# Optimization experiments

Measured on AMD Instinct MI355X. Metric: run time of the kernel, lower is better.

Reference implementation:

```python
import jax, jax.numpy as jnp
import numpy as np

MAX_SEQ_LEN = 4096

def bigbird_block_rand_mask(from_seq_length, to_seq_length, from_block_size, to_block_size, num_rand_blocks, last_idx=-1):
    rand_attn = np.zeros((from_seq_length // from_block_size - 2, num_rand_blocks), dtype=np.int32)
    middle_seq = np.arange(1, to_seq_length // to_block_size - 1, dtype=np.int32)
    last = to_seq_length // to_block_size - 1
    if last_idx > 2 * to_block_size:
        last = last_idx // to_block_size - 1
    r = num_rand_blocks
    nfb = from_seq_length // from_block_size
    for i in range(1, nfb - 1):
        start = i - 2
        end = i
        if i == 1:
            rand_attn[i - 1, :] = np.random.permutation(middle_seq[2:last])[:r]
        elif i == 2:
            rand_attn[i - 1, :] = np.random.permutation(middle_seq[3:last])[:r]
        elif i == nfb - 3:
            rand_attn[i - 1, :] = np.random.permutation(middle_seq[:last])[:r]
        elif i == nfb - 2:
            rand_attn[i - 1, :] = np.random.permutation(middle_seq[:last])[:r]
        elif start > last:
            start = last
            rand_attn[i - 1, :] = np.random.permutation(middle_seq[:start])[:r]
        elif end + 1 == last:
            rand_attn[i - 1, :] = np.random.permutation(middle_seq[:start])[:r]
        else:
            rand_attn[i - 1, :] = np.random.permutation(np.concatenate((middle_seq[:start], middle_seq[end + 1:last])))[:r]
    return rand_attn

def full_bigbird_mask(from_seq_length, to_seq_length, from_block_size, to_block_size, rand_attn):
    attn_mask = np.zeros((MAX_SEQ_LEN, MAX_SEQ_LEN), dtype=np.int32)
    for i in range(1, from_seq_length // from_block_size - 1):
        attn_mask[i * from_block_size:(i + 1) * from_block_size, (i - 1) * to_block_size:(i + 2) * to_block_size] = 1
        for j in rand_attn[i - 1, :]:
            attn_mask[i * from_block_size:(i + 1) * from_block_size, j * to_block_size:(j + 1) * to_block_size] = 1
    attn_mask[:from_block_size, :] = 1
    attn_mask[:, :to_block_size] = 1
    attn_mask[:, -to_block_size:] = 1
    attn_mask[-from_block_size:, :] = 1
    return attn_mask[:from_seq_length, :to_seq_length].astype(bool)

def setup_inputs() -> dict:
    B, H, F, T, D = 2, 16, 1024, 1024, 64
    BS, R, SEED = 64, 3, 0
    np.random.seed(SEED)
    rand_attn = np.stack([
        bigbird_block_rand_mask(MAX_SEQ_LEN, MAX_SEQ_LEN, BS, BS, R, last_idx=1024)[:F // BS - 2]
        for _ in range(H)
    ], axis=0)
    mask = np.stack([full_bigbird_mask(F, T, BS, BS, rand_attn[h]) for h in range(H)], axis=0)
    attention_mask = jnp.asarray(mask[None].astype(np.float32))  # [1, H, F, T]
    key = jax.random.key(0)
    kq, kk, kv = jax.random.split(key, 3)
    return {
        'query_layer': jax.random.normal(kq, (B, H, F, D), dtype=jnp.float32),
        'key_layer': jax.random.normal(kk, (B, H, T, D), dtype=jnp.float32),
        'value_layer': jax.random.normal(kv, (B, H, T, D), dtype=jnp.float32),
        'attention_mask': attention_mask,
    }

def reference(query_layer, key_layer, value_layer, attention_mask):
    d = query_layer.shape[-1]
    scores = jnp.einsum('bnfh,bnth->bnft', query_layer, key_layer) * (1.0 / np.sqrt(float(d)))
    scores = scores + (1.0 - attention_mask) * -10000.0
    probs = jax.nn.softmax(scores, axis=-1)
    # [batch, from_seq, heads, size_per_head]
    return jnp.einsum('bnft,bnth->bfnh', probs, value_layer)
```

## Files before the change

kernel.cpp:

```cpp
#include <hip/hip_runtime.h>

typedef __attribute__((ext_vector_type(4))) float f32x4;
typedef __attribute__((ext_vector_type(8))) short bf16x8;
typedef _Float16 f16x8 __attribute__((ext_vector_type(8)));

#define MFMA16(a, b, c) __builtin_amdgcn_mfma_f32_16x16x32_f16((a), (b), (c), 0, 0, 0)
#define MFMABF(a, b, c) __builtin_amdgcn_mfma_f32_16x16x32_bf16((a), (b), (c), 0, 0, 0)

constexpr size_t TILE_FRAG_BYTES = 8192;
constexpr size_t NTILES = 512;
constexpr size_t ARR_S  = NTILES * TILE_FRAG_BYTES;
constexpr size_t WS_NEED = 2 * ARR_S;

__device__ __forceinline__ int swz_off(int row, int col) {
    return (row * 128 + col * 2) ^ ((row & 7) << 4);
}
__device__ __forceinline__ f16x8 ld_frag16(const char* tile, int row, int col) {
    return *(const f16x8*)(tile + swz_off(row, col));
}

__global__ __launch_bounds__(256) void bigbird_prepass(
    const float* __restrict__ K, const float* __restrict__ V,
    char* __restrict__ ws) {
    __shared__ float vf[64][66];
    const int tile = blockIdx.x;
    const int tid  = threadIdx.x;
    const float* Kt = K + (size_t)tile * 4096;
    const float* Vt = V + (size_t)tile * 4096;
    f16x8* Ko = (f16x8*)(ws + (size_t)tile * TILE_FRAG_BYTES);
    f16x8* Vo = (f16x8*)(ws + ARR_S + (size_t)tile * TILE_FRAG_BYTES);

    {
        const int row = tid >> 2;
        const int c0  = (tid & 3) << 4;
        const float* p = Vt + row * 64 + c0;
        f32x4 e0 = *(const f32x4*)p,       e1 = *(const f32x4*)(p + 4),
              e2 = *(const f32x4*)(p + 8), e3 = *(const f32x4*)(p + 12);
#pragma unroll
        for (int e = 0; e < 4; ++e) {
            vf[row][c0 + e] = e0[e];     vf[row][c0 + 4 + e] = e1[e];
            vf[row][c0 + 8 + e] = e2[e]; vf[row][c0 + 12 + e] = e3[e];
        }
    }
#pragma unroll
    for (int t = 0; t < 2; ++t) {
        int s = tid + t * 256;
        int f = s >> 6, lane = s & 63;
        int j = f >> 1, kk = f & 1;
        int l16 = lane & 15, g = lane >> 4;
        const float* p = Kt + (j * 16 + l16) * 64 + kk * 32 + g * 8;
        f32x4 a = *(const f32x4*)p;
        f32x4 c = *(const f32x4*)(p + 4);
        f16x8 kv;
#pragma unroll
        for (int e = 0; e < 4; ++e) {
            kv[e]     = (_Float16)a[e];
            kv[4 + e] = (_Float16)c[e];
        }
        Ko[s] = kv;
    }
    __syncthreads();
#pragma unroll
    for (int t = 0; t < 2; ++t) {
        int s = tid + t * 256;
        int f = s >> 6, lane = s & 63;
        int j = f >> 1, kk = f & 1;
        int l16 = lane & 15, g = lane >> 4;
        f16x8 vv;
#pragma unroll
        for (int e = 0; e < 8; ++e)
            vv[e] = (_Float16)vf[kk * 32 + g * 8 + e][j * 16 + l16];
        Vo[s] = vv;
    }
}

__global__ __launch_bounds__(256, 2) void bigbird_main(
    const float* __restrict__ Q, const float* __restrict__ M,
    const char* __restrict__ ws, float* __restrict__ Out) {
    constexpr int H = 16, F = 1024, D = 64;

    __shared__ char fbuf[2][16384];
    __shared__ char p_sm[4][2048];
    __shared__ int flags[16];
    __shared__ int list[16];
    __shared__ int ncnt;

    const int i0  = blockIdx.x;
    const int xcd = i0 & 7;
    const int q0  = i0 >> 3;
    const int grp = xcd * 4 + (q0 >> 4);
    const int fb  = q0 & 15;
    const int b   = grp >> 4;
    const int h   = grp & 15;
    const int bh  = grp;

    const int tid  = threadIdx.x;
    const int lane = tid & 63;
    const int w    = tid >> 6;
    const int g    = lane >> 4;
    const int l16  = lane & 15;

    if (tid < 16)
        flags[tid] = (M[((size_t)(h * 1024 + fb * 64)) * 1024 + tid * 64] > 0.5f) ? 1 : 0;

    f16x8 qf[2];
    {
        const float* qr = Q + ((size_t)bh * F + fb * 64 + w * 16 + l16) * D;
#pragma unroll
        for (int kk = 0; kk < 2; ++kk) {
            const float* p = qr + kk * 32 + g * 8;
            f32x4 a = *(const f32x4*)p;
            f32x4 c = *(const f32x4*)(p + 4);
#pragma unroll
            for (int e = 0; e < 8; ++e)
                qf[kk][e] = (_Float16)((e < 4 ? a[e] : c[e - 4]) * 0.125f);
        }
    }
    __syncthreads();
    if (tid == 0) {
        int nn = 0;
        for (int t = 0; t < 16; ++t)
            if (flags[t]) list[nn++] = t;
        ncnt = nn;
    }
    __syncthreads();
    const int n = ncnt;

    f32x4 acc[4];
    float m_r[4], l_r[4];
#pragma unroll
    for (int j = 0; j < 4; ++j) acc[j] = f32x4{0.f, 0.f, 0.f, 0.f};
#pragma unroll
    for (int r = 0; r < 4; ++r) { m_r[r] = -1e30f; l_r[r] = 0.f; }

    const char* wsK = ws + (size_t)bh * 16 * TILE_FRAG_BYTES;
    const char* wsV = wsK + ARR_S;
    char* pw = p_sm[w];

    auto stage = [&](int bufi, int tb) {
        const char* Kt = wsK + (size_t)tb * TILE_FRAG_BYTES;
        const char* Vt = wsV + (size_t)tb * TILE_FRAG_BYTES;
        char* dst = fbuf[bufi] + w * 1024;
#pragma unroll
        for (int c = 0; c < 4; ++c) {
            const char* src = (c < 2 ? Kt + c * 4096 : Vt + (c - 2) * 4096) + tid * 16;
            __builtin_amdgcn_global_load_lds(
                (const __attribute__((address_space(1))) void*)src,
                (__attribute__((address_space(3))) void*)(dst + c * 4096), 16, 0, 0);
        }
    };

    if (n > 0) stage(0, list[0]);

    for (int i = 0; i < n; ++i) {
        __syncthreads();
        if (i + 1 < n) stage((i + 1) & 1, list[i + 1]);
        const char* Kb = fbuf[i & 1];
        const char* Vb = fbuf[i & 1] + 8192;

        f32x4 s[4];
#pragma unroll
        for (int j = 0; j < 4; ++j) {
            s[j] = f32x4{0.f, 0.f, 0.f, 0.f};
#pragma unroll
            for (int kk = 0; kk < 2; ++kk) {
                f16x8 kf = *(const f16x8*)(Kb + (j * 2 + kk) * 1024 + lane * 16);
                s[j] = MFMA16(qf[kk], kf, s[j]);
            }
        }

        float rmax[4];
#pragma unroll
        for (int r = 0; r < 4; ++r)
            rmax[r] = fmaxf(fmaxf(s[0][r], s[1][r]), fmaxf(s[2][r], s[3][r]));
#pragma unroll
        for (int off = 1; off < 16; off <<= 1)
#pragma unroll
            for (int r = 0; r < 4; ++r)
                rmax[r] = fmaxf(rmax[r], __shfl_xor(rmax[r], off, 64));
        float alpha[4], psum[4];
#pragma unroll
        for (int r = 0; r < 4; ++r) {
            float mn = fmaxf(m_r[r], rmax[r]);
            alpha[r] = __expf(m_r[r] - mn);
            m_r[r]   = mn;
            psum[r]  = 0.f;
        }
#pragma unroll
        for (int j = 0; j < 4; ++j)
#pragma unroll
            for (int r = 0; r < 4; ++r) {
                float pe = __expf(s[j][r] - m_r[r]);
                s[j][r] = pe;
                psum[r] += pe;
            }
#pragma unroll
        for (int off = 1; off < 16; off <<= 1)
#pragma unroll
            for (int r = 0; r < 4; ++r)
                psum[r] += __shfl_xor(psum[r], off, 64);
#pragma unroll
        for (int r = 0; r < 4; ++r)
            l_r[r] = l_r[r] * alpha[r] + psum[r];
#pragma unroll
        for (int j = 0; j < 4; ++j)
#pragma unroll
            for (int r = 0; r < 4; ++r)
                acc[j][r] *= alpha[r];

#pragma unroll
        for (int j = 0; j < 4; ++j)
#pragma unroll
            for (int r = 0; r < 4; ++r)
                *(_Float16*)(pw + swz_off(g * 4 + r, j * 16 + l16)) = (_Float16)s[j][r];
        asm volatile("s_waitcnt lgkmcnt(0)" ::: "memory");
        __builtin_amdgcn_sched_barrier(0);

#pragma unroll
        for (int kk = 0; kk < 2; ++kk) {
            f16x8 pa = ld_frag16(pw, l16, kk * 32 + g * 8);
#pragma unroll
            for (int jd = 0; jd < 4; ++jd) {
                f16x8 vfr = *(const f16x8*)(Vb + (jd * 2 + kk) * 1024 + lane * 16);
                acc[jd] = MFMA16(pa, vfr, acc[jd]);
            }
        }
    }

#pragma unroll
    for (int r = 0; r < 4; ++r) {
        float inv = 1.0f / l_r[r];
        int f = fb * 64 + w * 16 + g * 4 + r;
        float* ob = Out + ((size_t)(b * F + f) * H + h) * D;
#pragma unroll
        for (int jd = 0; jd < 4; ++jd)
            ob[jd * 16 + l16] = acc[jd][r] * inv;
    }
}

__device__ __forceinline__ unsigned short f2bf(float x) {
    unsigned u = __builtin_bit_cast(unsigned, x);
    unsigned r = u + 0x7fffu + ((u >> 16) & 1u);
    return (unsigned short)(r >> 16);
}
__device__ __forceinline__ float bf2f(unsigned short h) {
    return __builtin_bit_cast(float, (unsigned)h << 16);
}
__device__ __forceinline__ bf16x8 ld_fragb(const char* tile, int row, int col) {
    return *(const bf16x8*)(tile + swz_off(row, col));
}
__device__ __forceinline__ void stage_rm_fb(const float* __restrict__ src,
                                            char* hi_t, char* lo_t, float scale) {
    const int tid = threadIdx.x;
    const int row = tid >> 2;
    const int c0  = (tid & 3) << 4;
    const float* p = src + row * 64 + c0;
    f32x4 vv[4] = { *(const f32x4*)(p), *(const f32x4*)(p + 4),
                    *(const f32x4*)(p + 8), *(const f32x4*)(p + 12) };
    bf16x8 h2[2], l2[2];
#pragma unroll
    for (int e = 0; e < 16; ++e) {
        float x = vv[e >> 2][e & 3] * scale;
        unsigned short hb = f2bf(x);
        unsigned short lb = f2bf(x - bf2f(hb));
        h2[e >> 3][e & 7] = (short)hb;
        l2[e >> 3][e & 7] = (short)lb;
    }
#pragma unroll
    for (int gi = 0; gi < 2; ++gi) {
        int off = swz_off(row, c0 + gi * 8);
        *(bf16x8*)(hi_t + off) = h2[gi];
        *(bf16x8*)(lo_t + off) = l2[gi];
    }
}
__device__ __forceinline__ void stage_tr_fb(const float* __restrict__ src,
                                            char* hi_t, char* lo_t) {
    const int tid = threadIdx.x;
    const int t  = tid >> 2;
    const int c0 = (tid & 3) << 4;
    const float* p = src + t * 64 + c0;
    f32x4 vv[4] = { *(const f32x4*)(p), *(const f32x4*)(p + 4),
                    *(const f32x4*)(p + 8), *(const f32x4*)(p + 12) };
#pragma unroll
    for (int e = 0; e < 16; ++e) {
        float x = vv[e >> 2][e & 3];
        unsigned short hb = f2bf(x);
        unsigned short lb = f2bf(x - bf2f(hb));
        int d = c0 + e;
        int off = (d * 128 + t * 2) ^ ((d & 7) << 4);
        *(unsigned short*)(hi_t + off) = hb;
        *(unsigned short*)(lo_t + off) = lb;
    }
}
__global__ __launch_bounds__(256) void bigbird_kernel_fb(
    const float* __restrict__ Q, const float* __restrict__ K,
    const float* __restrict__ V, const float* __restrict__ M,
    float* __restrict__ Out) {
    constexpr int H = 16, F = 1024, D = 64;
    __shared__ char kq_hi[8192];
    __shared__ char kq_lo[8192];
    __shared__ char vt_hi[8192];
    __shared__ char vt_lo[8192];
    __shared__ char p_smf[8192];
    __shared__ int flags[16];
    const int bid = blockIdx.x;
    const int fb  = bid & 15;
    const int h   = (bid >> 4) & 15;
    const int b   = bid >> 8;
    const int tid  = threadIdx.x;
    const int lane = tid & 63;
    const int w    = tid >> 6;
    const int g    = lane >> 4;
    const int l16  = lane & 15;
    if (tid < 16)
        flags[tid] = (M[(h * 1024 + fb * 64) * 1024 + tid * 64] > 0.5f) ? 1 : 0;
    const float* qb = Q + ((size_t)(b * H + h) * F + fb * 64) * D;
    stage_rm_fb(qb, kq_hi, kq_lo, 0.125f);
    __syncthreads();
    bf16x8 qh[2], ql[2];
#pragma unroll
    for (int kk = 0; kk < 2; ++kk) {
        qh[kk] = ld_fragb(kq_hi, w * 16 + l16, kk * 32 + g * 8);
        ql[kk] = ld_fragb(kq_lo, w * 16 + l16, kk * 32 + g * 8);
    }
    f32x4 acc[4];
    float m_r[4], l_r[4];
#pragma unroll
    for (int j = 0; j < 4; ++j) acc[j] = f32x4{0.f, 0.f, 0.f, 0.f};
#pragma unroll
    for (int r = 0; r < 4; ++r) { m_r[r] = -1e30f; l_r[r] = 0.f; }
    const float* kb = K + (size_t)(b * H + h) * 1024 * D;
    const float* vb = V + (size_t)(b * H + h) * 1024 * D;
    for (int tb = 0; tb < 16; ++tb) {
        if (!flags[tb]) continue;
        __syncthreads();
        stage_rm_fb(kb + tb * 64 * D, kq_hi, kq_lo, 1.0f);
        stage_tr_fb(vb + tb * 64 * D, vt_hi, vt_lo);
        __syncthreads();
        f32x4 s[4];
#pragma unroll
        for (int j = 0; j < 4; ++j) {
            s[j] = f32x4{0.f, 0.f, 0.f, 0.f};
#pragma unroll
            for (int kk = 0; kk < 2; ++kk) {
                bf16x8 bhf = ld_fragb(kq_hi, j * 16 + l16, kk * 32 + g * 8);
                bf16x8 blf = ld_fragb(kq_lo, j * 16 + l16, kk * 32 + g * 8);
                s[j] = MFMABF(qh[kk], bhf, s[j]);
                s[j] = MFMABF(qh[kk], blf, s[j]);
                s[j] = MFMABF(ql[kk], bhf, s[j]);
            }
        }
        float rmax[4];
#pragma unroll
        for (int r = 0; r < 4; ++r)
            rmax[r] = fmaxf(fmaxf(s[0][r], s[1][r]), fmaxf(s[2][r], s[3][r]));
#pragma unroll
        for (int off = 1; off < 16; off <<= 1)
#pragma unroll
            for (int r = 0; r < 4; ++r)
                rmax[r] = fmaxf(rmax[r], __shfl_xor(rmax[r], off, 64));
        float alpha[4], psum[4];
#pragma unroll
        for (int r = 0; r < 4; ++r) {
            float mn = fmaxf(m_r[r], rmax[r]);
            alpha[r] = __expf(m_r[r] - mn);
            m_r[r]   = mn;
            psum[r]  = 0.f;
        }
#pragma unroll
        for (int j = 0; j < 4; ++j)
#pragma unroll
            for (int r = 0; r < 4; ++r) {
                float pe = __expf(s[j][r] - m_r[r]);
                s[j][r] = pe;
                psum[r] += pe;
            }
#pragma unroll
        for (int off = 1; off < 16; off <<= 1)
#pragma unroll
            for (int r = 0; r < 4; ++r)
                psum[r] += __shfl_xor(psum[r], off, 64);
#pragma unroll
        for (int r = 0; r < 4; ++r)
            l_r[r] = l_r[r] * alpha[r] + psum[r];
#pragma unroll
        for (int j = 0; j < 4; ++j)
#pragma unroll
            for (int r = 0; r < 4; ++r)
                acc[j][r] *= alpha[r];
#pragma unroll
        for (int j = 0; j < 4; ++j)
#pragma unroll
            for (int r = 0; r < 4; ++r) {
                int row = w * 16 + g * 4 + r;
                *(unsigned short*)(p_smf + swz_off(row, j * 16 + l16)) = f2bf(s[j][r]);
            }
        __syncthreads();
#pragma unroll
        for (int kk = 0; kk < 2; ++kk) {
            bf16x8 pa = ld_fragb(p_smf, w * 16 + l16, kk * 32 + g * 8);
#pragma unroll
            for (int jd = 0; jd < 4; ++jd) {
                bf16x8 vh = ld_fragb(vt_hi, jd * 16 + l16, kk * 32 + g * 8);
                bf16x8 vl = ld_fragb(vt_lo, jd * 16 + l16, kk * 32 + g * 8);
                acc[jd] = MFMABF(pa, vh, acc[jd]);
                acc[jd] = MFMABF(pa, vl, acc[jd]);
            }
        }
    }
#pragma unroll
    for (int r = 0; r < 4; ++r) {
        float inv = 1.0f / l_r[r];
        int f = fb * 64 + w * 16 + g * 4 + r;
        float* ob = Out + ((size_t)(b * F + f) * H + h) * D;
#pragma unroll
        for (int jd = 0; jd < 4; ++jd)
            ob[jd * 16 + l16] = acc[jd][r] * inv;
    }
}

extern "C" void kernel_launch(void* const* d_in, const int* in_sizes, int n_in,
                              void* d_out, int out_size, void* d_ws, size_t ws_size,
                              hipStream_t stream) {
    const float* q = (const float*)d_in[0];
    const float* k = (const float*)d_in[1];
    const float* v = (const float*)d_in[2];
    const float* m = (const float*)d_in[3];
    float* out = (float*)d_out;
    if (ws_size >= WS_NEED) {
        bigbird_prepass<<<dim3(512), dim3(256), 0, stream>>>(k, v, (char*)d_ws);
        bigbird_main<<<dim3(512), dim3(256), 0, stream>>>(q, m, (const char*)d_ws, out);
    } else {
        bigbird_kernel_fb<<<dim3(512), dim3(256), 0, stream>>>(q, k, v, m, out);
    }
}
```

Baseline: 44.82 us.

## Use two-pass softmax with direct global fragment loads instead of LDS staging

The main kernel drops the double-buffered LDS staging of K/V tiles and loads fragments straight from the workspace into registers. A first pass computes the exact row maximum over all active key blocks, and a second pass computes exponentials, sums and the PV product without online rescaling. Row-sum shuffles are deferred to the end, and the per-iteration block barriers are removed. The cost is reading K twice and losing async prefetch overlap, and the occupancy hint in launch bounds is relaxed.

After: 41.60 us. 7.2% less time.

```diff
diff --git a/kernel.cpp b/kernel.cpp
--- a/kernel.cpp
+++ b/kernel.cpp
@@ -74,12 +74,11 @@
     }
 }
 
-__global__ __launch_bounds__(256, 2) void bigbird_main(
+__global__ __launch_bounds__(256) void bigbird_main(
     const float* __restrict__ Q, const float* __restrict__ M,
     const char* __restrict__ ws, float* __restrict__ Out) {
     constexpr int H = 16, F = 1024, D = 64;
 
-    __shared__ char fbuf[2][16384];
     __shared__ char p_sm[4][2048];
     __shared__ int flags[16];
     __shared__ int list[16];
@@ -126,110 +125,101 @@
     __syncthreads();
     const int n = ncnt;
 
+    const f16x8* Kbase = (const f16x8*)ws + (size_t)bh * 16 * 512;
+    const f16x8* Vbase = (const f16x8*)(ws + ARR_S) + (size_t)bh * 16 * 512;
+    char* pw = p_sm[w];
+
+    float mrow[4];
+#pragma unroll
+    for (int r = 0; r < 4; ++r) mrow[r] = -1e30f;
+
+    for (int i = 0; i < n; ++i) {
+        const f16x8* Kf = Kbase + (size_t)list[i] * 512;
+        f16x8 kfr[4][2];
+#pragma unroll
+        for (int j = 0; j < 4; ++j)
+#pragma unroll
+            for (int kk = 0; kk < 2; ++kk)
+                kfr[j][kk] = Kf[(j * 2 + kk) * 64 + lane];
+        f32x4 sv[4];
+#pragma unroll
+        for (int j = 0; j < 4; ++j) {
+            sv[j] = f32x4{0.f, 0.f, 0.f, 0.f};
+#pragma unroll
+            for (int kk = 0; kk < 2; ++kk)
+                sv[j] = MFMA16(qf[kk], kfr[j][kk], sv[j]);
+        }
+#pragma unroll
+        for (int r = 0; r < 4; ++r)
+            mrow[r] = fmaxf(mrow[r],
+                      fmaxf(fmaxf(sv[0][r], sv[1][r]), fmaxf(sv[2][r], sv[3][r])));
+    }
+#pragma unroll
+    for (int off = 1; off < 16; off <<= 1)
+#pragma unroll
+        for (int r = 0; r < 4; ++r)
+            mrow[r] = fmaxf(mrow[r], __shfl_xor(mrow[r], off, 64));
+
     f32x4 acc[4];
-    float m_r[4], l_r[4];
+    float lsum[4];
 #pragma unroll
     for (int j = 0; j < 4; ++j) acc[j] = f32x4{0.f, 0.f, 0.f, 0.f};
 #pragma unroll
-    for (int r = 0; r < 4; ++r) { m_r[r] = -1e30f; l_r[r] = 0.f; }
-
-    const char* wsK = ws + (size_t)bh * 16 * TILE_FRAG_BYTES;
-    const char* wsV = wsK + ARR_S;
-    char* pw = p_sm[w];
-
-    auto stage = [&](int bufi, int tb) {
-        const char* Kt = wsK + (size_t)tb * TILE_FRAG_BYTES;
-        const char* Vt = wsV + (size_t)tb * TILE_FRAG_BYTES;
-        char* dst = fbuf[bufi] + w * 1024;
-#pragma unroll
-        for (int c = 0; c < 4; ++c) {
-            const char* src = (c < 2 ? Kt + c * 4096 : Vt + (c - 2) * 4096) + tid * 16;
-            __builtin_amdgcn_global_load_lds(
-                (const __attribute__((address_space(1))) void*)src,
-                (__attribute__((address_space(3))) void*)(dst + c * 4096), 16, 0, 0);
-        }
-    };
-
-    if (n > 0) stage(0, list[0]);
+    for (int r = 0; r < 4; ++r) lsum[r] = 0.f;
 
     for (int i = 0; i < n; ++i) {
-        __syncthreads();
-        if (i + 1 < n) stage((i + 1) & 1, list[i + 1]);
-        const char* Kb = fbuf[i & 1];
-        const char* Vb = fbuf[i & 1] + 8192;
-
-        f32x4 s[4];
+        const int tb = list[i];
+        const f16x8* Kf = Kbase + (size_t)tb * 512;
+        const f16x8* Vf = Vbase + (size_t)tb * 512;
+        f16x8 kfr[4][2], vfr[4][2];
+#pragma unroll
+        for (int j = 0; j < 4; ++j)
+#pragma unroll
+            for (int kk = 0; kk < 2; ++kk) {
+                kfr[j][kk] = Kf[(j * 2 + kk) * 64 + lane];
+                vfr[j][kk] = Vf[(j * 2 + kk) * 64 + lane];
+            }
+        f32x4 sv[4];
 #pragma unroll
         for (int j = 0; j < 4; ++j) {
-            s[j] = f32x4{0.f, 0.f, 0.f, 0.f};
-#pragma unroll
-            for (int kk = 0; kk < 2; ++kk) {
-                f16x8 kf = *(const f16x8*)(Kb + (j * 2 + kk) * 1024 + lane * 16);
-                s[j] = MFMA16(qf[kk], kf, s[j]);
-            }
-        }
-
-        float rmax[4];
-#pragma unroll
-        for (int r = 0; r < 4; ++r)
-            rmax[r] = fmaxf(fmaxf(s[0][r], s[1][r]), fmaxf(s[2][r], s[3][r]));
-#pragma unroll
-        for (int off = 1; off < 16; off <<= 1)
+            sv[j] = f32x4{0.f, 0.f, 0.f, 0.f};
+#pragma unroll
+            for (int kk = 0; kk < 2; ++kk)
+                sv[j] = MFMA16(qf[kk], kfr[j][kk], sv[j]);
+        }
+#pragma unroll
+        for (int j = 0; j < 4; ++j)
+#pragma unroll
+            for (int r = 0; r < 4; ++r) {
+                float pe = __expf(sv[j][r] - mrow[r]);
+                sv[j][r] = pe;
+                lsum[r] += pe;
+            }
+#pragma unroll
+        for (int j = 0; j < 4; ++j)
 #pragma unroll
             for (int r = 0; r < 4; ++r)
-                rmax[r] = fmaxf(rmax[r], __shfl_xor(rmax[r], off, 64));
-        float alpha[4], psum[4];
-#pragma unroll
-        for (int r = 0; r < 4; ++r) {
-            float mn = fmaxf(m_r[r], rmax[r]);
-            alpha[r] = __expf(m_r[r] - mn);
-            m_r[r]   = mn;
-            psum[r]  = 0.f;
-        }
-#pragma unroll
-        for (int j = 0; j < 4; ++j)
-#pragma unroll
-            for (int r = 0; r < 4; ++r) {
-                float pe = __expf(s[j][r] - m_r[r]);
-                s[j][r] = pe;
-                psum[r] += pe;
-            }
-#pragma unroll
-        for (int off = 1; off < 16; off <<= 1)
-#pragma unroll
-            for (int r = 0; r < 4; ++r)
-                psum[r] += __shfl_xor(psum[r], off, 64);
-#pragma unroll
-        for (int r = 0; r < 4; ++r)
-            l_r[r] = l_r[r] * alpha[r] + psum[r];
-#pragma unroll
-        for (int j = 0; j < 4; ++j)
-#pragma unroll
-            for (int r = 0; r < 4; ++r)
-                acc[j][r] *= alpha[r];
-
-#pragma unroll
-        for (int j = 0; j < 4; ++j)
-#pragma unroll
-            for (int r = 0; r < 4; ++r)
-                *(_Float16*)(pw + swz_off(g * 4 + r, j * 16 + l16)) = (_Float16)s[j][r];
+                *(_Float16*)(pw + swz_off(g * 4 + r, j * 16 + l16)) = (_Float16)sv[j][r];
         asm volatile("s_waitcnt lgkmcnt(0)" ::: "memory");
         __builtin_amdgcn_sched_barrier(0);
-
 #pragma unroll
         for (int kk = 0; kk < 2; ++kk) {
             f16x8 pa = ld_frag16(pw, l16, kk * 32 + g * 8);
 #pragma unroll
-            for (int jd = 0; jd < 4; ++jd) {
-                f16x8 vfr = *(const f16x8*)(Vb + (jd * 2 + kk) * 1024 + lane * 16);
-                acc[jd] = MFMA16(pa, vfr, acc[jd]);
-            }
-        }
-    }
+            for (int jd = 0; jd < 4; ++jd)
+                acc[jd] = MFMA16(pa, vfr[jd][kk], acc[jd]);
+        }
+    }
+
+#pragma unroll
+    for (int off = 1; off < 16; off <<= 1)
+#pragma unroll
+        for (int r = 0; r < 4; ++r)
+            lsum[r] += __shfl_xor(lsum[r], off, 64);
 
 #pragma unroll
     for (int r = 0; r < 4; ++r) {
-        float inv = 1.0f / l_r[r];
+        float inv = 1.0f / lsum[r];
         int f = fb * 64 + w * 16 + g * 4 + r;
         float* ob = Out + ((size_t)(b * F + f) * H + h) * D;
 #pragma unroll
```
